# Optimization experiments

Hardware: AMD Instinct MI355X
Metric: run time of the kernel (lower is better)

The kernel has to match this reference:

```python
import jax, jax.numpy as jnp
import numpy as np

# Spiking boolean gates on {0,1}-valued floats:
#   AND(a,b) = a*b ; OR(a,b) = a + b - a*b ; NOT(a) = 1 - a
#   XOR(a,b) = a + b - 2*a*b ; FullAdder: s = a^b^c, carry = a*b + c*(a^b)

def _xor(a, b):
    return a + b - 2.0 * a * b

def _or(a, b):
    return a + b - a * b


def setup_inputs() -> dict:
    key = jax.random.key(0)
    # FP64 bit patterns as 0/1 spikes; batch of 2M words -> 512 MB input
    x = jax.random.randint(key, (2_000_000, 64), 0, 2).astype(jnp.float32)
    return {"x": x}


def reference(x):
    ones = jnp.ones(x.shape[:-1] + (1,), x.dtype)
    # exponent bits (big-endian) -> little-endian
    e_le = jnp.flip(x[..., 1:12], axis=-1)  # [..., 11]
    # constant 1023 little-endian = ten 1s then a 0; NOT of it
    not_1023 = [0.0] * 10 + [1.0]
    # shift = e - 1023 via e + ~1023 + 1 (initial carry = 1)
    s_bits = []
    carry = ones
    for i in range(11):
        a = e_le[..., i:i + 1]
        b = not_1023[i]
        axb = _xor(a, b)
        s = _xor(axb, carry)
        carry = a * b + carry * axb
        s_bits.append(s)
    s_inv = [1.0 - s for s in s_bits]
    # high bits 3..10 all zero
    hi_zero = s_inv[3]
    for i in range(4, 11):
        hi_zero = hi_zero * s_inv[i]
    is_s = [
        hi_zero * (s_inv[0] * (s_inv[1] * s_inv[2])),   # shift == 0
        hi_zero * (s_bits[0] * (s_inv[1] * s_inv[2])),  # shift == 1
        hi_zero * (s_inv[0] * (s_bits[1] * s_inv[2])),  # shift == 2
        hi_zero * (s_bits[0] * (s_bits[1] * s_inv[2])), # shift == 3
        hi_zero * (s_inv[0] * (s_inv[1] * s_bits[2])),  # shift == 4
        hi_zero * (s_bits[0] * (s_inv[1] * s_bits[2])), # shift == 5
    ]
    m = [x[..., 12 + i:13 + i] for i in range(6)]  # top mantissa bits
    final_bits = []
    for b in range(6):
        terms = []
        for s in range(6):
            if s == b:
                terms.append(is_s[s] * ones)
            elif s > b and s - 1 - b < 6:
                terms.append(is_s[s] * m[s - 1 - b])
        res = terms[0]
        for t in terms[1:]:
            res = _or(res, t)
        final_bits.append(res)
    return jnp.concatenate(list(reversed(final_bits)), axis=-1)
```

## Files before the change

kernel.cpp:

```cpp
#include <hip/hip_runtime.h>

__global__ __launch_bounds__(256) void extract_low6_kernel(
    const float* __restrict__ x, float* __restrict__ out, int nrows) {
    int r = blockIdx.x * blockDim.x + threadIdx.x;
    if (r >= nrows) return;

    const float* row = x + (size_t)r * 64;
    float4 f0 = *(const float4*)(row);
    float4 f1 = *(const float4*)(row + 4);
    float4 f2 = *(const float4*)(row + 8);
    float4 f3 = *(const float4*)(row + 12);
    float2 f4 = *(const float2*)(row + 16);

    int e = 0;
    e |= (int)(f0.y != 0.f) << 10;
    e |= (int)(f0.z != 0.f) << 9;
    e |= (int)(f0.w != 0.f) << 8;
    e |= (int)(f1.x != 0.f) << 7;
    e |= (int)(f1.y != 0.f) << 6;
    e |= (int)(f1.z != 0.f) << 5;
    e |= (int)(f1.w != 0.f) << 4;
    e |= (int)(f2.x != 0.f) << 3;
    e |= (int)(f2.y != 0.f) << 2;
    e |= (int)(f2.z != 0.f) << 1;
    e |= (int)(f2.w != 0.f);

    int mant = 0;
    mant |= (int)(f3.x != 0.f) << 5;
    mant |= (int)(f3.y != 0.f) << 4;
    mant |= (int)(f3.z != 0.f) << 3;
    mant |= (int)(f3.w != 0.f) << 2;
    mant |= (int)(f4.x != 0.f) << 1;
    mant |= (int)(f4.y != 0.f);

    unsigned d = (unsigned)(e - 1023) & 2047u;
    int low6 = (d <= 5u) ? (((0x40 | mant) << d) >> 6) & 63 : 0;

    float2* o = (float2*)(out + (size_t)r * 6);
    o[0] = make_float2((float)((low6 >> 5) & 1), (float)((low6 >> 4) & 1));
    o[1] = make_float2((float)((low6 >> 3) & 1), (float)((low6 >> 2) & 1));
    o[2] = make_float2((float)((low6 >> 1) & 1), (float)(low6 & 1));
}

extern "C" void kernel_launch(void* const* d_in, const int* in_sizes, int n_in,
                              void* d_out, int out_size, void* d_ws, size_t ws_size,
                              hipStream_t stream) {
    const float* x = (const float*)d_in[0];
    float* out = (float*)d_out;
    int nrows = in_sizes[0] / 64;
    int block = 256;
    int grid = (nrows + block - 1) / block;
    extract_low6_kernel<<<grid, block, 0, stream>>>(x, out, nrows);
}
```

Baseline: 607.7 us.

## Stage row loads and output stores through shared memory for coalescing

Each block now loads the first 20 floats of its 256 rows cooperatively, with consecutive threads reading consecutive 16-byte chunks, and places them in LDS before each thread computes its row. The 6-float outputs are likewise gathered in LDS and written back as contiguous float4 stores. The aim is to replace strided per-thread row accesses with coalesced global traffic. In exchange it adds LDS usage, two barriers and integer divides, which may lower occupancy.

Measured after the change: 610.0 us. About the same (+0.4%).

```diff
diff --git a/kernel.cpp b/kernel.cpp
--- a/kernel.cpp
+++ b/kernel.cpp
@@ -1,45 +1,87 @@
 #include <hip/hip_runtime.h>
 
-__global__ __launch_bounds__(256) void extract_low6_kernel(
+
+#define BLOCK 256
+#define SLOTS 6
+
+__global__ __launch_bounds__(BLOCK) void extract_low6_kernel(
     const float* __restrict__ x, float* __restrict__ out, int nrows) {
-    int r = blockIdx.x * blockDim.x + threadIdx.x;
-    if (r >= nrows) return;
+    __shared__ float4 stage[BLOCK * SLOTS];
+    __shared__ float4 ostage4[BLOCK * 6 / 4];
+    float* ostage = (float*)ostage4;
 
-    const float* row = x + (size_t)r * 64;
-    float4 f0 = *(const float4*)(row);
-    float4 f1 = *(const float4*)(row + 4);
-    float4 f2 = *(const float4*)(row + 8);
-    float4 f3 = *(const float4*)(row + 12);
-    float2 f4 = *(const float2*)(row + 16);
+    const int t = threadIdx.x;
+    const long long row0 = (long long)blockIdx.x * BLOCK;
 
-    int e = 0;
-    e |= (int)(f0.y != 0.f) << 10;
-    e |= (int)(f0.z != 0.f) << 9;
-    e |= (int)(f0.w != 0.f) << 8;
-    e |= (int)(f1.x != 0.f) << 7;
-    e |= (int)(f1.y != 0.f) << 6;
-    e |= (int)(f1.z != 0.f) << 5;
-    e |= (int)(f1.w != 0.f) << 4;
-    e |= (int)(f2.x != 0.f) << 3;
-    e |= (int)(f2.y != 0.f) << 2;
-    e |= (int)(f2.z != 0.f) << 1;
-    e |= (int)(f2.w != 0.f);
+#pragma unroll
+    for (int k = 0; k < 5; ++k) {
+        int g = k * BLOCK + t;
+        int row = g / 5;
+        int c = g - row * 5;
+        if (row0 + row < nrows) {
+            stage[row * SLOTS + c] =
+                *(const float4*)(x + (((size_t)(row0 + row)) << 6) + (c << 2));
+        }
+    }
+    __syncthreads();
 
-    int mant = 0;
-    mant |= (int)(f3.x != 0.f) << 5;
-    mant |= (int)(f3.y != 0.f) << 4;
-    mant |= (int)(f3.z != 0.f) << 3;
-    mant |= (int)(f3.w != 0.f) << 2;
-    mant |= (int)(f4.x != 0.f) << 1;
-    mant |= (int)(f4.y != 0.f);
+    const bool valid = (row0 + t) < (long long)nrows;
+    int low6 = 0;
+    if (valid) {
+        float4 f0 = stage[t * SLOTS + 0];
+        float4 f1 = stage[t * SLOTS + 1];
+        float4 f2 = stage[t * SLOTS + 2];
+        float4 f3 = stage[t * SLOTS + 3];
+        float4 f4 = stage[t * SLOTS + 4];
 
-    unsigned d = (unsigned)(e - 1023) & 2047u;
-    int low6 = (d <= 5u) ? (((0x40 | mant) << d) >> 6) & 63 : 0;
+        int e = 0;
+        e |= (int)(f0.y != 0.f) << 10;
+        e |= (int)(f0.z != 0.f) << 9;
+        e |= (int)(f0.w != 0.f) << 8;
+        e |= (int)(f1.x != 0.f) << 7;
+        e |= (int)(f1.y != 0.f) << 6;
+        e |= (int)(f1.z != 0.f) << 5;
+        e |= (int)(f1.w != 0.f) << 4;
+        e |= (int)(f2.x != 0.f) << 3;
+        e |= (int)(f2.y != 0.f) << 2;
+        e |= (int)(f2.z != 0.f) << 1;
+        e |= (int)(f2.w != 0.f);
 
-    float2* o = (float2*)(out + (size_t)r * 6);
-    o[0] = make_float2((float)((low6 >> 5) & 1), (float)((low6 >> 4) & 1));
-    o[1] = make_float2((float)((low6 >> 3) & 1), (float)((low6 >> 2) & 1));
-    o[2] = make_float2((float)((low6 >> 1) & 1), (float)(low6 & 1));
+        int mant = 0;
+        mant |= (int)(f3.x != 0.f) << 5;
+        mant |= (int)(f3.y != 0.f) << 4;
+        mant |= (int)(f3.z != 0.f) << 3;
+        mant |= (int)(f3.w != 0.f) << 2;
+        mant |= (int)(f4.x != 0.f) << 1;
+        mant |= (int)(f4.y != 0.f);
+
+        unsigned d = (unsigned)(e - 1023) & 2047u;
+        low6 = (d <= 5u) ? (((0x40 | mant) << d) >> 6) & 63 : 0;
+
+        ostage[t * 6 + 0] = (float)((low6 >> 5) & 1);
+        ostage[t * 6 + 1] = (float)((low6 >> 4) & 1);
+        ostage[t * 6 + 2] = (float)((low6 >> 3) & 1);
+        ostage[t * 6 + 3] = (float)((low6 >> 2) & 1);
+        ostage[t * 6 + 4] = (float)((low6 >> 1) & 1);
+        ostage[t * 6 + 5] = (float)(low6 & 1);
+    }
+    __syncthreads();
+
+    const long long rem = (long long)nrows - row0;
+    if (rem >= BLOCK) {
+        float4* o4 = (float4*)(out + (size_t)row0 * 6);
+        const float4* s4 = (const float4*)ostage4;
+#pragma unroll
+        for (int base = 0; base < 384; base += BLOCK) {
+            int idx = base + t;
+            if (idx < 384) o4[idx] = s4[idx];
+        }
+    } else if (valid) {
+        float2* o = (float2*)(out + (size_t)(row0 + t) * 6);
+        o[0] = make_float2((float)((low6 >> 5) & 1), (float)((low6 >> 4) & 1));
+        o[1] = make_float2((float)((low6 >> 3) & 1), (float)((low6 >> 2) & 1));
+        o[2] = make_float2((float)((low6 >> 1) & 1), (float)(low6 & 1));
+    }
 }
 
 extern "C" void kernel_launch(void* const* d_in, const int* in_sizes, int n_in,
@@ -48,7 +90,6 @@
     const float* x = (const float*)d_in[0];
     float* out = (float*)d_out;
     int nrows = in_sizes[0] / 64;
-    int block = 256;
-    int grid = (nrows + block - 1) / block;
-    extract_low6_kernel<<<grid, block, 0, stream>>>(x, out, nrows);
+    int grid = (nrows + BLOCK - 1) / BLOCK;
+    extract_low6_kernel<<<grid, BLOCK, 0, stream>>>(x, out, nrows);
 }
```
